# Kernel optimization log

Hardware: AMD Instinct MI355X
Metric: run time of the kernel (lower is better)

Reference implementation:

```python
import jax, jax.numpy as jnp
import numpy as np

B, N, F = 32, 256, 12          # batch, Nc, in_dim
E_IN, E_H, E_OUT, N_OUT = 2 * (F + 1) + 6, 32, 30, 12


def setup_inputs() -> dict:
    key = jax.random.key(0)
    ks = jax.random.split(key, 12)
    x = jax.random.normal(ks[0], (B, N, F), jnp.float32)
    d = jax.random.uniform(ks[1], (B, N, N), jnp.float32, 0.1, 10.0)
    mask = jax.random.uniform(ks[2], (B, N, N)) > 0.3
    adj_dist = jnp.where(mask, d, 0.0)
    adj_direct = jax.random.uniform(ks[3], (B, N, N), jnp.float32, 0.0, 2.0 * np.pi)
    wind_mean = jax.random.normal(ks[4], (B, 2), jnp.float32)
    wind_std = jax.random.uniform(ks[5], (B, 2), jnp.float32, 0.5, 1.5)
    s = 0.1
    W1 = jax.random.normal(ks[6], (E_IN, E_H), jnp.float32) * s
    b1 = jnp.zeros((E_H,), jnp.float32)
    W2 = jax.random.normal(ks[7], (E_H, E_OUT), jnp.float32) * s
    b2 = jnp.zeros((E_OUT,), jnp.float32)
    W3 = jax.random.normal(ks[8], (E_OUT, N_OUT), jnp.float32) * s
    b3 = jnp.zeros((N_OUT,), jnp.float32)
    return {"x": x, "adj_dist": adj_dist, "adj_direct": adj_direct,
            "wind_mean": wind_mean, "wind_std": wind_std,
            "W1": W1, "b1": b1, "W2": W2, "b2": b2, "W3": W3, "b3": b3}


def reference(x, adj_dist, adj_direct, wind_mean, wind_std, W1, b1, W2, b2, W3, b3):
    # adj mask: edge exists where adj_dist != 0  -> (B,N,N,1)
    a = (adj_dist != 0).astype(x.dtype)[..., None]
    # broadcast-gather src/target node features onto all pairs, masked, +edge flag
    node_src = jnp.concatenate([a * x[:, :, None, :], a], axis=-1)   # (B,N,N,F+1)
    node_tgt = jnp.concatenate([a * x[:, None, :, :], a], axis=-1)   # (B,N,N,F+1)
    # normalize dist/direction over (batch, src) dims; torch .std is unbiased
    dist = adj_dist[..., None]
    direc = adj_direct[..., None]
    dist_n = (dist - dist.mean(axis=(0, 1))) / dist.std(axis=(0, 1), ddof=1)
    direc_n = (direc - direc.mean(axis=(0, 1))) / direc.std(axis=(0, 1), ddof=1)
    # edge feature tensor (B,N,N,32) = 2*(F+1) + 6
    out0 = jnp.concatenate(
        [node_src, node_tgt, dist_n, a, direc_n, a, a, a], axis=-1)
    # tiny edge MLP (sigmoid-sigmoid)
    h = jax.nn.sigmoid(out0 @ W1 + b1)
    e = jax.nn.sigmoid(h @ W2 + b2)                                  # (B,N,N,E_OUT)
    # aggregate: sum over src rows (incoming) minus sum over dest cols (outgoing)
    agg = e.sum(axis=1) - e.sum(axis=2)                              # (B,N,E_OUT)
    # node MLP
    return jax.nn.sigmoid(agg @ W3 + b3)                             # (B,N,N_OUT)
```

## Files before the change

kernel.cpp:

```cpp
#include <hip/hip_runtime.h>
#include <hip/hip_bf16.h>
#include <math.h>

#define BB 32
#define NN 256
#define FF 12
#define WS_SUMS   0
#define WS_STATS  1024
#define WS_W2P    2048
#define WS_B2P    3072
#define WS_USG    4096
#define WS_UTPG   266240
#define WS_MIN    528384
#define WS_PLUS   1052672

typedef __attribute__((ext_vector_type(8))) short bf16x8;
typedef __attribute__((ext_vector_type(4))) float f32x4;

__device__ __forceinline__ float sig(float x) {
    return __builtin_amdgcn_rcpf(1.0f + __expf(-x));
}
__device__ __forceinline__ short f2bf(float x) {
    __hip_bfloat16 b = __float2bfloat16(x);
    short s; __builtin_memcpy(&s, &b, 2); return s;
}
__device__ __forceinline__ float bf2f(short s) {
    __hip_bfloat16 b; __builtin_memcpy(&b, &s, 2);
    return __bfloat162float(b);
}
__device__ __forceinline__ unsigned pkbf(float lo, float hi) {
    unsigned ulo, uhi;
    __builtin_memcpy(&ulo, &lo, 4); __builtin_memcpy(&uhi, &hi, 4);
    return (uhi & 0xffff0000u) | (ulo >> 16);
}

__global__ __launch_bounds__(256) void colstats_kernel(
    const float* __restrict__ dist, const float* __restrict__ direc, float* __restrict__ sums)
{
    const int t = threadIdx.x;
    const int r0 = blockIdx.x * 32;
    float sd = 0.f, sdd = 0.f, sr = 0.f, srr = 0.f;
#pragma unroll 4
    for (int rr = 0; rr < 32; ++rr) {
        const float d  = dist [(r0 + rr) * NN + t];
        const float dr = direc[(r0 + rr) * NN + t];
        sd += d;  sdd = fmaf(d, d, sdd);
        sr += dr; srr = fmaf(dr, dr, srr);
    }
    atomicAdd(&sums[t],        sd);
    atomicAdd(&sums[256 + t],  sdd);
    atomicAdd(&sums[512 + t],  sr);
    atomicAdd(&sums[768 + t],  srr);
}

__global__ __launch_bounds__(256) void finalize_kernel(
    const float* __restrict__ sums, const float* __restrict__ W2, const float* __restrict__ b2,
    float* __restrict__ stats, float* __restrict__ W2p, float* __restrict__ b2p)
{
    const int t = threadIdx.x;
    const float M = (float)(BB * NN);
    {   const float s = sums[t], q = sums[256 + t];
        const float mean = s / M;
        float var = (q - s * mean) / (M - 1.0f);
        if (var < 1e-20f) var = 1e-20f;
        stats[t] = mean; stats[256 + t] = rsqrtf(var);
    }
    {   const float s = sums[512 + t], q = sums[768 + t];
        const float mean = s / M;
        float var = (q - s * mean) / (M - 1.0f);
        if (var < 1e-20f) var = 1e-20f;
        stats[512 + t] = mean; stats[768 + t] = rsqrtf(var);
    }
    for (int idx = t; idx < 1024; idx += 256) {
        const int k = idx >> 5, m = idx & 31;
        W2p[idx] = (m < 30) ? W2[k * 30 + m] : 0.0f;
    }
    if (t < 32) b2p[t] = (t < 30) ? b2[t] : 0.0f;
}

__global__ __launch_bounds__(256) void node_pre_kernel(
    const float* __restrict__ x, const float* __restrict__ W1, const float* __restrict__ b1,
    float* __restrict__ usg, float* __restrict__ utpg)
{
    const int idx = blockIdx.x * 256 + threadIdx.x;
    const int r = idx >> 5, k = idx & 31;
    const float* xr = x + r * FF;
    float us = 0.f, ut = 0.f;
#pragma unroll
    for (int f = 0; f < FF; ++f) {
        const float xv = xr[f];
        us = fmaf(xv, W1[f * 32 + k], us);
        ut = fmaf(xv, W1[(13 + f) * 32 + k], ut);
    }
    const float ca = W1[12 * 32 + k] + W1[25 * 32 + k] + W1[27 * 32 + k]
                   + W1[29 * 32 + k] + W1[30 * 32 + k] + W1[31 * 32 + k];
    usg[idx]  = us;
    utpg[idx] = ut + ca + b1[k];
}

__global__ __launch_bounds__(256, 4) void edge_mfma_kernel(
    const float* __restrict__ adj_dist, const float* __restrict__ adj_direct,
    const float* __restrict__ W1, const float* __restrict__ b1,
    const float* __restrict__ usg, const float* __restrict__ utpg,
    const float* __restrict__ stats, const float* __restrict__ W2p,
    const float* __restrict__ b2p, float* __restrict__ plus,
    float* __restrict__ minusv, int lognit)
{
    __shared__ float us_s[64][32];
    __shared__ float pool[8192];
    float (*mins)[4][32] = reinterpret_cast<float(*)[4][32]>(pool);
    float (*ldst)[129]   = reinterpret_cast<float(*)[129]>(pool);

    const int t    = threadIdx.x;
    const int nit  = 1 << lognit;
    const int R    = NN >> lognit;
    const int bid  = blockIdx.x;
    const int b    = bid >> (lognit + 1);
    const int it   = (bid >> 1) & (nit - 1);
    const int jh   = bid & 1;
    const int i0   = it * R;
    const int w    = t >> 6;
    const int l    = t & 63;
    const int m0   = l & 15;
    const int g    = l >> 4;
    const int kb   = g << 3;
    const int jbase = (jh << 7) + (w << 5);

    { const int k = t & 31;
      for (int ii = t >> 5; ii < R; ii += 8)
          us_s[ii][k] = usg[((b << 8) + i0 + ii) * 32 + k]; }
    __syncthreads();

    float b1c[8], r26c[8], r28c[8];
#pragma unroll
    for (int e = 0; e < 8; ++e) {
        b1c[e]  = b1[kb + e];
        r26c[e] = W1[26 * 32 + kb + e];
        r28c[e] = W1[28 * 32 + kb + e];
    }
    float utpc[2][8];
#pragma unroll
    for (int jt = 0; jt < 2; ++jt) {
        const int j = jbase + (jt << 4) + m0;
        const float4* uv = (const float4*)(utpg + ((b << 8) + j) * 32 + kb);
        float4 a0 = uv[0], a1 = uv[1];
        utpc[jt][0]=a0.x; utpc[jt][1]=a0.y; utpc[jt][2]=a0.z; utpc[jt][3]=a0.w;
        utpc[jt][4]=a1.x; utpc[jt][5]=a1.y; utpc[jt][6]=a1.z; utpc[jt][7]=a1.w;
    }
    float mdp[2], isdp[2], mrp[2], isrp[2];
#pragma unroll
    for (int jt = 0; jt < 2; ++jt) {
        const int j = jbase + (jt << 4) + m0;
        mdp[jt] = stats[j];        isdp[jt] = stats[256 + j];
        mrp[jt] = stats[512 + j];  isrp[jt] = stats[768 + j];
    }
    bf16x8 whi[2], wlo[2];
#pragma unroll
    for (int mt = 0; mt < 2; ++mt) {
        const int m = m0 + (mt << 4);
#pragma unroll
        for (int e = 0; e < 8; ++e) {
            const float wv = W2p[(kb + e) * 32 + m];
            const short h16 = f2bf(wv);
            whi[mt][e] = h16;
            wlo[mt][e] = f2bf(wv - bf2f(h16));
        }
    }
    const float b2c[2] = { b2p[m0], b2p[m0 + 16] };
    const bool mt1ok = (m0 < 14);

    float accp[2][2][4];
#pragma unroll
    for (int jt = 0; jt < 2; ++jt)
#pragma unroll
        for (int mt = 0; mt < 2; ++mt)
#pragma unroll
            for (int r = 0; r < 4; ++r) accp[jt][mt][r] = 0.0f;

    const int col = (jh << 7) + (w << 5) + (l & 31);
    const float* dptr = adj_dist   + (((b << 8) + i0) << 8) + col;
    const float* rptr = adj_direct + (((b << 8) + i0) << 8) + col;
    float dN = dptr[0], rN = rptr[0];

#pragma unroll 1
    for (int i = 0; i < R; ++i) {
        const float dcur = dN, rcur = rN;
        if (i + 1 < R) { dN = dptr[(i + 1) << 8]; rN = rptr[(i + 1) << 8]; }

        float usc[8];
        { const float4* uv = (const float4*)&us_s[i][kb];
          float4 a0 = uv[0], a1 = uv[1];
          usc[0]=a0.x; usc[1]=a0.y; usc[2]=a0.z; usc[3]=a0.w;
          usc[4]=a1.x; usc[5]=a1.y; usc[6]=a1.z; usc[7]=a1.w; }

        bf16x8 afr[2];
#pragma unroll
        for (int jt = 0; jt < 2; ++jt) {
            const int src = (jt << 4) + m0;
            const float dv = __shfl(dcur, src);
            const float rv = __shfl(rcur, src);
            const bool  a  = (dv != 0.0f);
            const float dn = (dv - mdp[jt]) * isdp[jt];
            const float rn = (rv - mrp[jt]) * isrp[jt];
            float h[8];
#pragma unroll
            for (int e = 0; e < 8; ++e) {
                float z = a ? (usc[e] + utpc[jt][e]) : b1c[e];
                z = fmaf(dn, r26c[e], z);
                z = fmaf(rn, r28c[e], z);
                h[e] = sig(z);
            }
            union { bf16x8 v; unsigned u[4]; } af;
#pragma unroll
            for (int p = 0; p < 4; ++p) af.u[p] = pkbf(h[2*p], h[2*p+1]);
            afr[jt] = af.v;
        }

        float msum0 = 0.0f, msum1 = 0.0f;
#pragma unroll
        for (int jt = 0; jt < 2; ++jt) {
#pragma unroll
            for (int mt = 0; mt < 2; ++mt) {
                f32x4 d4 = { b2c[mt], b2c[mt], b2c[mt], b2c[mt] };
                d4 = __builtin_amdgcn_mfma_f32_16x16x32_bf16(afr[jt], wlo[mt], d4, 0, 0, 0);
                d4 = __builtin_amdgcn_mfma_f32_16x16x32_bf16(afr[jt], whi[mt], d4, 0, 0, 0);
#pragma unroll
                for (int r = 0; r < 4; ++r) {
                    float e = sig(d4[r]);
                    if (mt == 1 && !mt1ok) e = 0.0f;
                    accp[jt][mt][r] += e;
                    if (mt == 0) msum0 += e; else msum1 += e;
                }
            }
        }
        msum0 += __shfl_xor(msum0, 16); msum0 += __shfl_xor(msum0, 32);
        msum1 += __shfl_xor(msum1, 16); msum1 += __shfl_xor(msum1, 32);
        if (l < 16) { mins[i][w][l] = msum0; mins[i][w][l + 16] = msum1; }
    }
    __syncthreads();

    { const int m = t & 31;
      if (m < 30)
          for (int ii = t >> 5; ii < R; ii += 8) {
              const float s = mins[ii][0][m] + mins[ii][1][m]
                            + mins[ii][2][m] + mins[ii][3][m];
              minusv[((b * 2 + jh) * 32 + m) * 256 + i0 + ii] = s;
          } }
    __syncthreads();

#pragma unroll
    for (int jt = 0; jt < 2; ++jt)
#pragma unroll
        for (int mt = 0; mt < 2; ++mt) {
            const int m = m0 + (mt << 4);
            if (m < 30) {
#pragma unroll
                for (int r = 0; r < 4; ++r) {
                    const int jl = (w << 5) + (jt << 4) + (g << 2) + r;
                    ldst[m][jl] = accp[jt][mt][r];
                }
            }
        }
    __syncthreads();
    { const int base = ((b << lognit) + it) << 13;
      const int jl = t & 127;
#pragma unroll
      for (int mi = 0; mi < 15; ++mi) {
          const int m = (mi << 1) + (t >> 7);
          plus[base + (m << 8) + (jh << 7) + jl] = ldst[m][jl];
      }
    }
}

__global__ __launch_bounds__(256) void reduce_out_kernel(
    const float* __restrict__ plus, const float* __restrict__ minusv,
    const float* __restrict__ W3, const float* __restrict__ b3,
    float* __restrict__ out, int lognit)
{
    __shared__ float agg_s[32][33];
    const int b   = blockIdx.x >> 3;
    const int nh  = blockIdx.x & 7;
    const int t   = threadIdx.x;
    const int nl  = t & 31;
    const int n   = (nh << 5) + nl;
    const int mg  = t >> 5;
    const int nit = 1 << lognit;

    float acc[4] = {0.f, 0.f, 0.f, 0.f};
#pragma unroll 1
    for (int it = 0; it < nit; ++it) {
        const float* p = plus + (((b << lognit) + it) << 13) + n;
#pragma unroll
        for (int q = 0; q < 4; ++q) acc[q] += p[((mg << 2) + q) << 8];
    }
#pragma unroll
    for (int q = 0; q < 4; ++q) {
        const int m = (mg << 2) + q;
        float v = acc[q]
                - minusv[((b * 2 + 0) * 32 + m) * 256 + n]
                - minusv[((b * 2 + 1) * 32 + m) * 256 + n];
        agg_s[nl][m] = (m < 30) ? v : 0.0f;
    }
    __syncthreads();

    for (int task = t; task < 384; task += 256) {
        const int n2 = task / 12, o = task % 12;
        float z = b3[o];
#pragma unroll
        for (int m = 0; m < 30; ++m) z = fmaf(agg_s[n2][m], W3[m * 12 + o], z);
        out[(((b << 8) + (nh << 5) + n2) * 12) + o] = sig(z);
    }
}

extern "C" void kernel_launch(void* const* d_in, const int* in_sizes, int n_in,
                              void* d_out, int out_size, void* d_ws, size_t ws_size,
                              hipStream_t stream)
{
    const float* x    = (const float*)d_in[0];
    const float* adjd = (const float*)d_in[1];
    const float* adjr = (const float*)d_in[2];
    const float* W1   = (const float*)d_in[5];
    const float* b1   = (const float*)d_in[6];
    const float* W2   = (const float*)d_in[7];
    const float* b2   = (const float*)d_in[8];
    const float* W3   = (const float*)d_in[9];
    const float* b3   = (const float*)d_in[10];
    float* ws  = (float*)d_ws;
    float* out = (float*)d_out;

    int lognit = 2;
    if      (ws_size >= ((size_t)WS_PLUS + 16u * 262144u) * 4u) lognit = 4;
    else if (ws_size >= ((size_t)WS_PLUS +  8u * 262144u) * 4u) lognit = 3;

    hipMemsetAsync(ws + WS_SUMS, 0, 1024 * sizeof(float), stream);

    colstats_kernel<<<256, 256, 0, stream>>>(adjd, adjr, ws + WS_SUMS);
    node_pre_kernel<<<1024, 256, 0, stream>>>(x, W1, b1, ws + WS_USG, ws + WS_UTPG);
    finalize_kernel<<<1, 256, 0, stream>>>(ws + WS_SUMS, W2, b2,
                                           ws + WS_STATS, ws + WS_W2P, ws + WS_B2P);
    edge_mfma_kernel<<<BB << (lognit + 1), 256, 0, stream>>>(adjd, adjr, W1, b1,
                                                             ws + WS_USG, ws + WS_UTPG,
                                                             ws + WS_STATS, ws + WS_W2P,
                                                             ws + WS_B2P, ws + WS_PLUS,
                                                             ws + WS_MIN, lognit);
    reduce_out_kernel<<<BB * 8, 256, 0, stream>>>(ws + WS_PLUS, ws + WS_MIN,
                                                  W3, b3, out, lognit);
}
```

Before: 149.8 us.

## Merge prep kernels, drop atomics, shrink edge tiles and transpose partial outputs

Merges the column-statistics and node-precompute kernels into one launch, which removes the memset and the atomics. Per-block partial sums are written out and reduced by a multi-block finalize kernel. The edge kernel now gives each wave 16 columns instead of 32, launches four column quarters per row chunk, reads source-node terms straight from global memory instead of LDS, and raises occupancy to 8 blocks per CU. The plus and minus partials are stored node-major so the final reduce can use vector loads. The cost is more partial buffers in the workspace and more redundant per-block setup in the edge kernel.

New measurement: 324.5 us. +116.6%, slower.

```diff
diff --git a/kernel.cpp b/kernel.cpp
--- a/kernel.cpp
+++ b/kernel.cpp
@@ -5,14 +5,14 @@
 #define BB 32
 #define NN 256
 #define FF 12
-#define WS_SUMS   0
-#define WS_STATS  1024
-#define WS_W2P    2048
-#define WS_B2P    3072
-#define WS_USG    4096
-#define WS_UTPG   266240
-#define WS_MIN    528384
-#define WS_PLUS   1052672
+#define WS_PART   0
+#define WS_STATS  262144
+#define WS_W2P    263168
+#define WS_B2P    264192
+#define WS_USG    264256
+#define WS_UTPG   526400
+#define WS_MIN    788544
+#define WS_PLUS   1837120
 
 typedef __attribute__((ext_vector_type(8))) short bf16x8;
 typedef __attribute__((ext_vector_type(4))) float f32x4;
@@ -34,102 +34,111 @@
     return (uhi & 0xffff0000u) | (ulo >> 16);
 }
 
-__global__ __launch_bounds__(256) void colstats_kernel(
-    const float* __restrict__ dist, const float* __restrict__ direc, float* __restrict__ sums)
+__global__ __launch_bounds__(256) void pre_kernel(
+    const float* __restrict__ dist, const float* __restrict__ direc,
+    const float* __restrict__ x, const float* __restrict__ W1,
+    const float* __restrict__ b1, float* __restrict__ partial,
+    float* __restrict__ usg, float* __restrict__ utpg)
 {
     const int t = threadIdx.x;
-    const int r0 = blockIdx.x * 32;
-    float sd = 0.f, sdd = 0.f, sr = 0.f, srr = 0.f;
+    if (blockIdx.x < 256) {
+        const int r0 = blockIdx.x * 32;
+        float sd = 0.f, sdd = 0.f, sr = 0.f, srr = 0.f;
 #pragma unroll 4
-    for (int rr = 0; rr < 32; ++rr) {
-        const float d  = dist [(r0 + rr) * NN + t];
-        const float dr = direc[(r0 + rr) * NN + t];
-        sd += d;  sdd = fmaf(d, d, sdd);
-        sr += dr; srr = fmaf(dr, dr, srr);
-    }
-    atomicAdd(&sums[t],        sd);
-    atomicAdd(&sums[256 + t],  sdd);
-    atomicAdd(&sums[512 + t],  sr);
-    atomicAdd(&sums[768 + t],  srr);
+        for (int rr = 0; rr < 32; ++rr) {
+            const float d  = dist [(r0 + rr) * NN + t];
+            const float dr = direc[(r0 + rr) * NN + t];
+            sd += d;  sdd = fmaf(d, d, sdd);
+            sr += dr; srr = fmaf(dr, dr, srr);
+        }
+        float* p = partial + blockIdx.x * 1024;
+        p[t] = sd; p[256 + t] = sdd; p[512 + t] = sr; p[768 + t] = srr;
+    } else {
+        const int idx = (blockIdx.x - 256) * 256 + t;
+        const int r = idx >> 5, k = idx & 31;
+        const float* xr = x + r * FF;
+        float us = 0.f, ut = 0.f;
+#pragma unroll
+        for (int f = 0; f < FF; ++f) {
+            const float xv = xr[f];
+            us = fmaf(xv, W1[f * 32 + k], us);
+            ut = fmaf(xv, W1[(13 + f) * 32 + k], ut);
+        }
+        const float ca = W1[12 * 32 + k] + W1[25 * 32 + k] + W1[27 * 32 + k]
+                       + W1[29 * 32 + k] + W1[30 * 32 + k] + W1[31 * 32 + k];
+        usg[idx]  = us;
+        utpg[idx] = ut + ca + b1[k];
+    }
 }
 
 __global__ __launch_bounds__(256) void finalize_kernel(
-    const float* __restrict__ sums, const float* __restrict__ W2, const float* __restrict__ b2,
-    float* __restrict__ stats, float* __restrict__ W2p, float* __restrict__ b2p)
+    const float* __restrict__ partial, const float* __restrict__ W2,
+    const float* __restrict__ b2, float* __restrict__ stats,
+    float* __restrict__ W2p, float* __restrict__ b2p)
 {
     const int t = threadIdx.x;
-    const float M = (float)(BB * NN);
-    {   const float s = sums[t], q = sums[256 + t];
-        const float mean = s / M;
-        float var = (q - s * mean) / (M - 1.0f);
-        if (var < 1e-20f) var = 1e-20f;
-        stats[t] = mean; stats[256 + t] = rsqrtf(var);
-    }
-    {   const float s = sums[512 + t], q = sums[768 + t];
-        const float mean = s / M;
-        float var = (q - s * mean) / (M - 1.0f);
-        if (var < 1e-20f) var = 1e-20f;
-        stats[512 + t] = mean; stats[768 + t] = rsqrtf(var);
-    }
-    for (int idx = t; idx < 1024; idx += 256) {
-        const int k = idx >> 5, m = idx & 31;
-        W2p[idx] = (m < 30) ? W2[k * 30 + m] : 0.0f;
-    }
-    if (t < 32) b2p[t] = (t < 30) ? b2[t] : 0.0f;
-}
-
-__global__ __launch_bounds__(256) void node_pre_kernel(
-    const float* __restrict__ x, const float* __restrict__ W1, const float* __restrict__ b1,
-    float* __restrict__ usg, float* __restrict__ utpg)
-{
-    const int idx = blockIdx.x * 256 + threadIdx.x;
-    const int r = idx >> 5, k = idx & 31;
-    const float* xr = x + r * FF;
-    float us = 0.f, ut = 0.f;
-#pragma unroll
-    for (int f = 0; f < FF; ++f) {
-        const float xv = xr[f];
-        us = fmaf(xv, W1[f * 32 + k], us);
-        ut = fmaf(xv, W1[(13 + f) * 32 + k], ut);
-    }
-    const float ca = W1[12 * 32 + k] + W1[25 * 32 + k] + W1[27 * 32 + k]
-                   + W1[29 * 32 + k] + W1[30 * 32 + k] + W1[31 * 32 + k];
-    usg[idx]  = us;
-    utpg[idx] = ut + ca + b1[k];
-}
-
-__global__ __launch_bounds__(256, 4) void edge_mfma_kernel(
+    if (blockIdx.x == 8) {
+        for (int idx = t; idx < 1024; idx += 256) {
+            const int k = idx >> 5, m = idx & 31;
+            W2p[idx] = (m < 30) ? W2[k * 30 + m] : 0.0f;
+        }
+        if (t < 32) b2p[t] = (t < 30) ? b2[t] : 0.0f;
+        return;
+    }
+    __shared__ float red[4][8][32];
+    const int jl = t & 31;
+    const int c  = t >> 5;
+    const int j  = blockIdx.x * 32 + jl;
+    float s0 = 0.f, s1 = 0.f, s2 = 0.f, s3 = 0.f;
+    for (int bk = c; bk < 256; bk += 8) {
+        const float* p = partial + bk * 1024;
+        s0 += p[j]; s1 += p[256 + j]; s2 += p[512 + j]; s3 += p[768 + j];
+    }
+    red[0][c][jl] = s0; red[1][c][jl] = s1; red[2][c][jl] = s2; red[3][c][jl] = s3;
+    __syncthreads();
+    if (t < 32) {
+        float a0 = 0.f, a1 = 0.f, a2 = 0.f, a3 = 0.f;
+#pragma unroll
+        for (int cc = 0; cc < 8; ++cc) {
+            a0 += red[0][cc][t]; a1 += red[1][cc][t];
+            a2 += red[2][cc][t]; a3 += red[3][cc][t];
+        }
+        const float M = (float)(BB * NN);
+        const int jj = blockIdx.x * 32 + t;
+        {   const float mean = a0 / M;
+            float var = (a1 - a0 * mean) / (M - 1.0f);
+            if (var < 1e-20f) var = 1e-20f;
+            stats[jj] = mean; stats[256 + jj] = rsqrtf(var); }
+        {   const float mean = a2 / M;
+            float var = (a3 - a2 * mean) / (M - 1.0f);
+            if (var < 1e-20f) var = 1e-20f;
+            stats[512 + jj] = mean; stats[768 + jj] = rsqrtf(var); }
+    }
+}
+
+__global__ __launch_bounds__(256, 8) void edge_mfma_kernel(
     const float* __restrict__ adj_dist, const float* __restrict__ adj_direct,
     const float* __restrict__ W1, const float* __restrict__ b1,
     const float* __restrict__ usg, const float* __restrict__ utpg,
     const float* __restrict__ stats, const float* __restrict__ W2p,
-    const float* __restrict__ b2p, float* __restrict__ plus,
+    const float* __restrict__ b2p, float* __restrict__ plusT,
     float* __restrict__ minusv, int lognit)
 {
-    __shared__ float us_s[64][32];
-    __shared__ float pool[8192];
-    float (*mins)[4][32] = reinterpret_cast<float(*)[4][32]>(pool);
-    float (*ldst)[129]   = reinterpret_cast<float(*)[129]>(pool);
-
-    const int t    = threadIdx.x;
-    const int nit  = 1 << lognit;
-    const int R    = NN >> lognit;
-    const int bid  = blockIdx.x;
-    const int b    = bid >> (lognit + 1);
-    const int it   = (bid >> 1) & (nit - 1);
-    const int jh   = bid & 1;
-    const int i0   = it * R;
-    const int w    = t >> 6;
-    const int l    = t & 63;
-    const int m0   = l & 15;
-    const int g    = l >> 4;
-    const int kb   = g << 3;
-    const int jbase = (jh << 7) + (w << 5);
-
-    { const int k = t & 31;
-      for (int ii = t >> 5; ii < R; ii += 8)
-          us_s[ii][k] = usg[((b << 8) + i0 + ii) * 32 + k]; }
-    __syncthreads();
+    __shared__ float mins[32][4][32];
+
+    const int t   = threadIdx.x;
+    const int R   = NN >> lognit;
+    const int jq  = blockIdx.x & 3;
+    const int bit = blockIdx.x >> 2;
+    const int b   = bit >> lognit;
+    const int it  = bit & ((1 << lognit) - 1);
+    const int i0  = it * R;
+    const int w   = t >> 6;
+    const int l   = t & 63;
+    const int m0  = l & 15;
+    const int g   = l >> 4;
+    const int kb  = g << 3;
+    const int j   = (jq << 6) + (w << 4) + m0;
 
     float b1c[8], r26c[8], r28c[8];
 #pragma unroll
@@ -138,22 +147,14 @@
         r26c[e] = W1[26 * 32 + kb + e];
         r28c[e] = W1[28 * 32 + kb + e];
     }
-    float utpc[2][8];
-#pragma unroll
-    for (int jt = 0; jt < 2; ++jt) {
-        const int j = jbase + (jt << 4) + m0;
-        const float4* uv = (const float4*)(utpg + ((b << 8) + j) * 32 + kb);
-        float4 a0 = uv[0], a1 = uv[1];
-        utpc[jt][0]=a0.x; utpc[jt][1]=a0.y; utpc[jt][2]=a0.z; utpc[jt][3]=a0.w;
-        utpc[jt][4]=a1.x; utpc[jt][5]=a1.y; utpc[jt][6]=a1.z; utpc[jt][7]=a1.w;
-    }
-    float mdp[2], isdp[2], mrp[2], isrp[2];
-#pragma unroll
-    for (int jt = 0; jt < 2; ++jt) {
-        const int j = jbase + (jt << 4) + m0;
-        mdp[jt] = stats[j];        isdp[jt] = stats[256 + j];
-        mrp[jt] = stats[512 + j];  isrp[jt] = stats[768 + j];
-    }
+    float utpc[8];
+    { const float4* uv = (const float4*)(utpg + ((b << 8) + j) * 32 + kb);
+      const float4 a0 = uv[0], a1 = uv[1];
+      utpc[0]=a0.x; utpc[1]=a0.y; utpc[2]=a0.z; utpc[3]=a0.w;
+      utpc[4]=a1.x; utpc[5]=a1.y; utpc[6]=a1.z; utpc[7]=a1.w; }
+    const float md  = stats[j],       isd = stats[256 + j];
+    const float mr  = stats[512 + j], isr = stats[768 + j];
+
     bf16x8 whi[2], wlo[2];
 #pragma unroll
     for (int mt = 0; mt < 2; ++mt) {
@@ -169,68 +170,54 @@
     const float b2c[2] = { b2p[m0], b2p[m0 + 16] };
     const bool mt1ok = (m0 < 14);
 
-    float accp[2][2][4];
-#pragma unroll
-    for (int jt = 0; jt < 2; ++jt)
-#pragma unroll
-        for (int mt = 0; mt < 2; ++mt)
-#pragma unroll
-            for (int r = 0; r < 4; ++r) accp[jt][mt][r] = 0.0f;
-
-    const int col = (jh << 7) + (w << 5) + (l & 31);
-    const float* dptr = adj_dist   + (((b << 8) + i0) << 8) + col;
-    const float* rptr = adj_direct + (((b << 8) + i0) << 8) + col;
+    float accp[2][4];
+#pragma unroll
+    for (int mt = 0; mt < 2; ++mt)
+#pragma unroll
+        for (int r = 0; r < 4; ++r) accp[mt][r] = 0.0f;
+
+    const float* dptr  = adj_dist   + (((b << 8) + i0) << 8) + j;
+    const float* rptr  = adj_direct + (((b << 8) + i0) << 8) + j;
+    const float* usrow = usg + ((b << 8) + i0) * 32 + kb;
     float dN = dptr[0], rN = rptr[0];
 
 #pragma unroll 1
     for (int i = 0; i < R; ++i) {
-        const float dcur = dN, rcur = rN;
+        const float dv = dN, rv = rN;
         if (i + 1 < R) { dN = dptr[(i + 1) << 8]; rN = rptr[(i + 1) << 8]; }
 
-        float usc[8];
-        { const float4* uv = (const float4*)&us_s[i][kb];
-          float4 a0 = uv[0], a1 = uv[1];
-          usc[0]=a0.x; usc[1]=a0.y; usc[2]=a0.z; usc[3]=a0.w;
-          usc[4]=a1.x; usc[5]=a1.y; usc[6]=a1.z; usc[7]=a1.w; }
-
-        bf16x8 afr[2];
-#pragma unroll
-        for (int jt = 0; jt < 2; ++jt) {
-            const int src = (jt << 4) + m0;
-            const float dv = __shfl(dcur, src);
-            const float rv = __shfl(rcur, src);
-            const bool  a  = (dv != 0.0f);
-            const float dn = (dv - mdp[jt]) * isdp[jt];
-            const float rn = (rv - mrp[jt]) * isrp[jt];
-            float h[8];
-#pragma unroll
-            for (int e = 0; e < 8; ++e) {
-                float z = a ? (usc[e] + utpc[jt][e]) : b1c[e];
-                z = fmaf(dn, r26c[e], z);
-                z = fmaf(rn, r28c[e], z);
-                h[e] = sig(z);
-            }
-            union { bf16x8 v; unsigned u[4]; } af;
-#pragma unroll
-            for (int p = 0; p < 4; ++p) af.u[p] = pkbf(h[2*p], h[2*p+1]);
-            afr[jt] = af.v;
-        }
+        const float4 u0 = *(const float4*)(usrow + i * 32);
+        const float4 u1 = *(const float4*)(usrow + i * 32 + 4);
+        const float usc[8] = {u0.x,u0.y,u0.z,u0.w,u1.x,u1.y,u1.z,u1.w};
+
+        const bool  a  = (dv != 0.0f);
+        const float dn = (dv - md) * isd;
+        const float rn = (rv - mr) * isr;
+
+        float h[8];
+#pragma unroll
+        for (int e = 0; e < 8; ++e) {
+            float z = a ? (usc[e] + utpc[e]) : b1c[e];
+            z = fmaf(dn, r26c[e], z);
+            z = fmaf(rn, r28c[e], z);
+            h[e] = sig(z);
+        }
+        union { bf16x8 v; unsigned u[4]; } af;
+#pragma unroll
+        for (int p = 0; p < 4; ++p) af.u[p] = pkbf(h[2*p], h[2*p+1]);
 
         float msum0 = 0.0f, msum1 = 0.0f;
 #pragma unroll
-        for (int jt = 0; jt < 2; ++jt) {
-#pragma unroll
-            for (int mt = 0; mt < 2; ++mt) {
-                f32x4 d4 = { b2c[mt], b2c[mt], b2c[mt], b2c[mt] };
-                d4 = __builtin_amdgcn_mfma_f32_16x16x32_bf16(afr[jt], wlo[mt], d4, 0, 0, 0);
-                d4 = __builtin_amdgcn_mfma_f32_16x16x32_bf16(afr[jt], whi[mt], d4, 0, 0, 0);
-#pragma unroll
-                for (int r = 0; r < 4; ++r) {
-                    float e = sig(d4[r]);
-                    if (mt == 1 && !mt1ok) e = 0.0f;
-                    accp[jt][mt][r] += e;
-                    if (mt == 0) msum0 += e; else msum1 += e;
-                }
+        for (int mt = 0; mt < 2; ++mt) {
+            f32x4 d4 = { b2c[mt], b2c[mt], b2c[mt], b2c[mt] };
+            d4 = __builtin_amdgcn_mfma_f32_16x16x32_bf16(af.v, wlo[mt], d4, 0, 0, 0);
+            d4 = __builtin_amdgcn_mfma_f32_16x16x32_bf16(af.v, whi[mt], d4, 0, 0, 0);
+#pragma unroll
+            for (int r = 0; r < 4; ++r) {
+                float e = sig(d4[r]);
+                if (mt == 1 && !mt1ok) e = 0.0f;
+                accp[mt][r] += e;
+                if (mt == 0) msum0 += e; else msum1 += e;
             }
         }
         msum0 += __shfl_xor(msum0, 16); msum0 += __shfl_xor(msum0, 32);
@@ -239,68 +226,49 @@
     }
     __syncthreads();
 
-    { const int m = t & 31;
-      if (m < 30)
-          for (int ii = t >> 5; ii < R; ii += 8) {
-              const float s = mins[ii][0][m] + mins[ii][1][m]
-                            + mins[ii][2][m] + mins[ii][3][m];
-              minusv[((b * 2 + jh) * 32 + m) * 256 + i0 + ii] = s;
-          } }
-    __syncthreads();
-
-#pragma unroll
-    for (int jt = 0; jt < 2; ++jt)
-#pragma unroll
-        for (int mt = 0; mt < 2; ++mt) {
-            const int m = m0 + (mt << 4);
-            if (m < 30) {
-#pragma unroll
-                for (int r = 0; r < 4; ++r) {
-                    const int jl = (w << 5) + (jt << 4) + (g << 2) + r;
-                    ldst[m][jl] = accp[jt][mt][r];
-                }
-            }
-        }
-    __syncthreads();
-    { const int base = ((b << lognit) + it) << 13;
-      const int jl = t & 127;
-#pragma unroll
-      for (int mi = 0; mi < 15; ++mi) {
-          const int m = (mi << 1) + (t >> 7);
-          plus[base + (m << 8) + (jh << 7) + jl] = ldst[m][jl];
+    for (int idx = t; idx < (R << 5); idx += 256) {
+        const int ii = idx >> 5, m = idx & 31;
+        const float s = mins[ii][0][m] + mins[ii][1][m]
+                      + mins[ii][2][m] + mins[ii][3][m];
+        minusv[((((b << 2) + jq) << 8) + i0 + ii) * 32 + m] = s;
+    }
+
+    { float* pT = plusT + ((size_t)((b << lognit) + it) << 13);
+#pragma unroll
+      for (int mt = 0; mt < 2; ++mt) {
+          const int m = m0 + (mt << 4);
+#pragma unroll
+          for (int r = 0; r < 4; ++r) {
+              const int jo = (jq << 6) + (w << 4) + (g << 2) + r;
+              pT[jo * 32 + m] = accp[mt][r];
+          }
       }
     }
 }
 
 __global__ __launch_bounds__(256) void reduce_out_kernel(
-    const float* __restrict__ plus, const float* __restrict__ minusv,
+    const float* __restrict__ plusT, const float* __restrict__ minusv,
     const float* __restrict__ W3, const float* __restrict__ b3,
     float* __restrict__ out, int lognit)
 {
-    __shared__ float agg_s[32][33];
+    __shared__ float agg_s[32][36];
     const int b   = blockIdx.x >> 3;
     const int nh  = blockIdx.x & 7;
     const int t   = threadIdx.x;
     const int nl  = t & 31;
+    const int mq  = t >> 5;
     const int n   = (nh << 5) + nl;
-    const int mg  = t >> 5;
     const int nit = 1 << lognit;
 
-    float acc[4] = {0.f, 0.f, 0.f, 0.f};
+    f32x4 acc = {0.f, 0.f, 0.f, 0.f};
 #pragma unroll 1
-    for (int it = 0; it < nit; ++it) {
-        const float* p = plus + (((b << lognit) + it) << 13) + n;
-#pragma unroll
-        for (int q = 0; q < 4; ++q) acc[q] += p[((mg << 2) + q) << 8];
-    }
-#pragma unroll
-    for (int q = 0; q < 4; ++q) {
-        const int m = (mg << 2) + q;
-        float v = acc[q]
-                - minusv[((b * 2 + 0) * 32 + m) * 256 + n]
-                - minusv[((b * 2 + 1) * 32 + m) * 256 + n];
-        agg_s[nl][m] = (m < 30) ? v : 0.0f;
-    }
+    for (int itb = 0; itb < nit; ++itb)
+        acc += *(const f32x4*)(plusT + ((size_t)((b << lognit) + itb) << 13)
+                               + n * 32 + (mq << 2));
+#pragma unroll
+    for (int jq = 0; jq < 4; ++jq)
+        acc -= *(const f32x4*)(minusv + ((((b << 2) + jq) << 8) + n) * 32 + (mq << 2));
+    *(f32x4*)&agg_s[nl][mq << 2] = acc;
     __syncthreads();
 
     for (int task = t; task < 384; task += 256) {
@@ -328,21 +296,17 @@
     float* ws  = (float*)d_ws;
     float* out = (float*)d_out;
 
-    int lognit = 2;
-    if      (ws_size >= ((size_t)WS_PLUS + 16u * 262144u) * 4u) lognit = 4;
-    else if (ws_size >= ((size_t)WS_PLUS +  8u * 262144u) * 4u) lognit = 3;
-
-    hipMemsetAsync(ws + WS_SUMS, 0, 1024 * sizeof(float), stream);
-
-    colstats_kernel<<<256, 256, 0, stream>>>(adjd, adjr, ws + WS_SUMS);
-    node_pre_kernel<<<1024, 256, 0, stream>>>(x, W1, b1, ws + WS_USG, ws + WS_UTPG);
-    finalize_kernel<<<1, 256, 0, stream>>>(ws + WS_SUMS, W2, b2,
+    int lognit = 4;
+    if (ws_size < ((size_t)WS_PLUS + 16u * 262144u) * 4u) lognit = 3;
+
+    pre_kernel<<<1280, 256, 0, stream>>>(adjd, adjr, x, W1, b1,
+                                         ws + WS_PART, ws + WS_USG, ws + WS_UTPG);
+    finalize_kernel<<<9, 256, 0, stream>>>(ws + WS_PART, W2, b2,
                                            ws + WS_STATS, ws + WS_W2P, ws + WS_B2P);
-    edge_mfma_kernel<<<BB << (lognit + 1), 256, 0, stream>>>(adjd, adjr, W1, b1,
-                                                             ws + WS_USG, ws + WS_UTPG,
-                                                             ws + WS_STATS, ws + WS_W2P,
-                                                             ws + WS_B2P, ws + WS_PLUS,
-                                                             ws + WS_MIN, lognit);
+    edge_mfma_kernel<<<(BB << lognit) << 2, 256, 0, stream>>>(
+        adjd, adjr, W1, b1, ws + WS_USG, ws + WS_UTPG,
+        ws + WS_STATS, ws + WS_W2P, ws + WS_B2P,
+        ws + WS_PLUS, ws + WS_MIN, lognit);
     reduce_out_kernel<<<BB * 8, 256, 0, stream>>>(ws + WS_PLUS, ws + WS_MIN,
                                                   W3, b3, out, lognit);
 }
```
